# Kernel tuning notes

Measured on AMD Instinct MI355X. Metric: run time of the kernel, lower is better.

The kernel has to match this reference:

```python
import jax, jax.numpy as jnp
import numpy as np

D = 4096
K = 128
N = 8192
EPS = 1e-6


def setup_inputs() -> dict:
    key = jax.random.key(0)
    k1, k2 = jax.random.split(key)
    x = jax.random.normal(k1, (N, D), dtype=jnp.float32)
    # theta = [W (d*K), mu (d), sigma (d), alpha (K)]; sigma/alpha must be positive
    theta = jax.random.uniform(k2, (D * K + 2 * D + K,), dtype=jnp.float32)
    return {"x": x, "theta": theta, "full_data_size": 100000}


def reference(x, theta, full_data_size):
    W = theta[: D * K].reshape(D, K)
    mu = theta[D * K : D * K + D]
    sigma = theta[D * K + D : D * K + 2 * D]
    alpha = theta[D * K + 2 * D :]

    # W_multiplied = W * alpha (broadcast over columns)
    Wm = W * alpha  # [D, K]
    # var_noise = sigma * eye(D) + eps : diag(sigma) plus eps added to EVERY entry
    cov = Wm @ Wm.T + jnp.diag(sigma) + EPS  # [D, D]

    L = jnp.linalg.cholesky(cov)  # [D, D], lower
    diff = x - mu  # [N, D]
    # Solve L y = diff^T for all samples at once
    y = jax.scipy.linalg.solve_triangular(L, diff.T, lower=True)  # [D, N]
    quad = jnp.sum(y * y, axis=0)  # [N]
    logdet = 2.0 * jnp.sum(jnp.log(jnp.diagonal(L)))
    log2pi = jnp.float32(np.log(2.0 * np.pi))
    logp = -0.5 * (D * log2pi + logdet + quad)  # [N]

    n = x.shape[0]
    return jnp.sum(logp) * (full_data_size / n)
```

## Files before the change

### kernel.cpp

```cpp
#include <hip/hip_runtime.h>
#include <math.h>

#define D 4096
#define K 128
#define KP 129
#define NC 144
#define NROWS 8192
#define QS 144
#define MS 132
#define NP 132
#define NPS 136
#define NB 12
#define NPAN (NP / NB)
#define MSPLIT 6
#define LOG2PI 1.8378770664093453

typedef __attribute__((ext_vector_type(8))) short bh8;
typedef __attribute__((ext_vector_type(4))) float f32x4;

__device__ __forceinline__ unsigned short f2bf(float f) {
  unsigned int u = __float_as_uint(f);
  unsigned int r = u + 0x7FFFu + ((u >> 16) & 1u);
  return (unsigned short)(r >> 16);
}
__device__ __forceinline__ float bf2f(unsigned short u) {
  return __uint_as_float(((unsigned int)u) << 16);
}
__device__ __forceinline__ float blo(unsigned int v) { return __uint_as_float(v << 16); }
__device__ __forceinline__ float bhi(unsigned int v) { return __uint_as_float(v & 0xFFFF0000u); }

__device__ __forceinline__ float blockReduceSum256(float v) {
  #pragma unroll
  for (int off = 32; off > 0; off >>= 1) v += __shfl_down(v, off, 64);
  __shared__ float tmp[4];
  __syncthreads();
  if ((threadIdx.x & 63) == 0) tmp[threadIdx.x >> 6] = v;
  __syncthreads();
  float r = 0.0f;
  if (threadIdx.x == 0) r = tmp[0] + tmp[1] + tmp[2] + tmp[3];
  return r;
}

__global__ __launch_bounds__(256) void k_prep(const float* __restrict__ theta,
                                              unsigned short* __restrict__ VbT) {
  int c = blockIdx.x;
  const float* sg = theta + (size_t)D * K + D;
  float al = (c < K) ? theta[(size_t)D * K + 2 * D + c] : 0.0f;
  for (int d = threadIdx.x; d < D; d += 256) {
    float v;
    if (c < K)       v = theta[(size_t)d * K + c] * al / sg[d];
    else if (c == K) v = 1.0e-3f / sg[d];
    else             v = 0.0f;
    VbT[(size_t)c * D + d] = f2bf(v);
  }
}

__global__ __launch_bounds__(256) void k_M(const float* __restrict__ theta,
                                           const unsigned short* __restrict__ VbT,
                                           float* __restrict__ M) {
  int j = blockIdx.x, kk2 = blockIdx.y;
  if (kk2 < j) return;
  const float* sg = theta + (size_t)D * K + D;
  float acc = 0.0f;
  for (int d0 = threadIdx.x * 8; d0 < D; d0 += 2048) {
    uint4 ua = *reinterpret_cast<const uint4*>(&VbT[(size_t)j * D + d0]);
    uint4 ub = *reinterpret_cast<const uint4*>(&VbT[(size_t)kk2 * D + d0]);
    float4 s0 = *reinterpret_cast<const float4*>(&sg[d0]);
    float4 s1 = *reinterpret_cast<const float4*>(&sg[d0 + 4]);
    acc += s0.x * blo(ua.x) * blo(ub.x) + s0.y * bhi(ua.x) * bhi(ub.x)
         + s0.z * blo(ua.y) * blo(ub.y) + s0.w * bhi(ua.y) * bhi(ub.y)
         + s1.x * blo(ua.z) * blo(ub.z) + s1.y * bhi(ua.z) * bhi(ub.z)
         + s1.z * blo(ua.w) * blo(ub.w) + s1.w * bhi(ua.w) * bhi(ub.w);
  }
  float r = blockReduceSum256(acc);
  if (threadIdx.x == 0) {
    float m = r + (j == kk2 ? 1.0f : 0.0f);
    M[j * MS + kk2] = m;
    M[kk2 * MS + j] = m;
  }
}

__global__ __launch_bounds__(256) void k_small(const float* __restrict__ theta,
                                               const unsigned short* __restrict__ VbT,
                                               const float* __restrict__ colsum,
                                               const float* __restrict__ colsumsq,
                                               float* __restrict__ tvec,
                                               float* __restrict__ mvec,
                                               float* __restrict__ scalars) {
  int b = blockIdx.x;
  if (b < 2 * KP) {
    int c = (b >= KP) ? b - KP : b;
    const float* src = (b >= KP) ? (theta + (size_t)D * K) : colsum;
    float a = 0.0f;
    for (int d = threadIdx.x; d < D; d += 256) a += bf2f(VbT[(size_t)c * D + d]) * src[d];
    float r = blockReduceSum256(a);
    if (threadIdx.x == 0) { if (b < KP) tvec[c] = r; else mvec[c] = r; }
  } else {
    const float* mu = theta + (size_t)D * K;
    const float* sg = theta + (size_t)D * K + D;
    float a = 0.0f, bb = 0.0f;
    for (int d = threadIdx.x; d < D; d += 256) {
      float s = sg[d];
      float m = mu[d];
      a += logf(s);
      bb += (colsumsq[d] - 2.0f * m * colsum[d] + (float)NROWS * m * m) / s;
    }
    float ra = blockReduceSum256(a);
    float rb = blockReduceSum256(bb);
    if (threadIdx.x == 0) { scalars[0] = ra; scalars[1] = rb; }
  }
}

#define GBM 32
#define GBK 128
#define NSTEP (D / GBK)
#define XSS 136
#define GEMM_BLOCKS (NROWS / GBM)
#define CS_BLOCKS 32
#define CS_ROWS (NROWS / CS_BLOCKS)

struct CholSh {
  float A[NP][NPS];
  float G[NP][NPS];
  float Tst[NPAN][NB][NB + 1];
};
struct GemmSh {
  unsigned short Xs[GBM][XSS];
  unsigned short Vs[NC][XSS];
};
union ParSh {
  CholSh c;
  GemmSh g;
};

__device__ void chol_body(CholSh& sh, const float* __restrict__ Mg,
                          float* __restrict__ Gg, float* __restrict__ scalars) {
  auto& A = sh.A;
  auto& G = sh.G;
  auto& Tst = sh.Tst;
  __shared__ float redB[16];
  int tid = threadIdx.x;

  if (tid == 0) scalars[3] = 0.0f;
  for (int idx = tid; idx < NP * NP; idx += 1024) {
    int r = idx / NP, c = idx - r * NP;
    A[r][c] = (r < KP && c < KP) ? Mg[r * MS + c] : (r == c ? 1.0f : 0.0f);
  }
  __syncthreads();

  for (int p = 0; p < NPAN; ++p) {
    int j0 = p * NB, j1 = j0 + NB;
    int nbrows = NP - j1;
    int nG = p * NB;
    if (tid < 128) {
      float T[NB][NB];
      #pragma unroll
      for (int r = 0; r < NB; ++r)
        #pragma unroll
        for (int c = 0; c <= r; ++c)
          T[r][c] = A[j0 + r][j0 + c];
      float dinv[NB];
      #pragma unroll
      for (int jj = 0; jj < NB; ++jj) {
        float dv = sqrtf(T[jj][jj]);
        float iv = 1.0f / dv;
        dinv[jj] = iv;
        #pragma unroll
        for (int r = jj + 1; r < NB; ++r) T[r][jj] *= iv;
        #pragma unroll
        for (int cc = jj + 1; cc < NB; ++cc)
          #pragma unroll
          for (int r = cc; r < NB; ++r)
            T[r][cc] -= T[r][jj] * T[cc][jj];
      }
      #pragma unroll
      for (int r = 0; r < NB; ++r) {
        float tmp[NB];
        #pragma unroll
        for (int c = 0; c < r; ++c) {
          float s = 0.0f;
          #pragma unroll
          for (int k = c; k < r; ++k) s += T[r][k] * T[k][c];
          tmp[c] = -s * dinv[r];
        }
        #pragma unroll
        for (int c = 0; c < r; ++c) T[r][c] = tmp[c];
        T[r][r] = dinv[r];
      }
      if (tid == 0) {
        #pragma unroll
        for (int r = 0; r < NB; ++r) {
          float g[NB];
          #pragma unroll
          for (int c = 0; c < NB; ++c) g[c] = (c <= r) ? T[r][c] : 0.0f;
          float4* dst = reinterpret_cast<float4*>(&G[j0 + r][j0]);
          float4 g0 = {g[0], g[1], g[2], g[3]};
          float4 g1 = {g[4], g[5], g[6], g[7]};
          float4 g2 = {g[8], g[9], g[10], g[11]};
          dst[0] = g0; dst[1] = g1; dst[2] = g2;
        }
      }
      if (tid < nbrows) {
        int r = j1 + tid;
        float* arow = &A[r][j0];
        float4 q0 = *reinterpret_cast<const float4*>(arow);
        float4 q1 = *reinterpret_cast<const float4*>(arow + 4);
        float4 q2 = *reinterpret_cast<const float4*>(arow + 8);
        float ro[NB] = {q0.x, q0.y, q0.z, q0.w, q1.x, q1.y, q1.z, q1.w,
                        q2.x, q2.y, q2.z, q2.w};
        float rn[NB];
        #pragma unroll
        for (int cc = 0; cc < NB; ++cc) {
          float s = 0.0f;
          #pragma unroll
          for (int k = 0; k <= cc; ++k) s += ro[k] * T[cc][k];
          rn[cc] = s;
        }
        float4 w0 = {rn[0], rn[1], rn[2], rn[3]};
        float4 w1 = {rn[4], rn[5], rn[6], rn[7]};
        float4 w2 = {rn[8], rn[9], rn[10], rn[11]};
        *reinterpret_cast<float4*>(arow) = w0;
        *reinterpret_cast<float4*>(arow + 4) = w1;
        *reinterpret_cast<float4*>(arow + 8) = w2;
      }
    } else if (tid < 128 + MSPLIT * nG) {
      int t2 = tid - 128;
      int q = t2 / (NB * MSPLIT);
      int rem = t2 - q * (NB * MSPLIT);
      int j = rem % NB, mg = rem / NB;
      int qI = q * NB;
      int m0 = mg * 2;
      float t0 = 0.0f, t1 = 0.0f;
      for (int k = q; k < p; ++k) {
        int kI = k * NB;
        #pragma unroll
        for (int n = 0; n < NB; ++n) {
          float g = G[kI + n][qI + j];
          t0 += A[j0 + m0 + 0][kI + n] * g;
          t1 += A[j0 + m0 + 1][kI + n] * g;
        }
      }
      Tst[q][m0 + 0][j] = t0;
      Tst[q][m0 + 1][j] = t1;
    }
    __syncthreads();
    if (tid < nG) {
      int q = tid / NB, j = tid - (tid / NB) * NB;
      int qI = q * NB;
      float w[NB];
      #pragma unroll
      for (int m = 0; m < NB; ++m) w[m] = Tst[q][m][j];
      #pragma unroll
      for (int i = 0; i < NB; ++i) {
        float s = 0.0f;
        #pragma unroll
        for (int m = 0; m <= i; ++m) s += G[j0 + i][j0 + m] * w[m];
        G[j0 + i][qI + j] = -s;
      }
    } else {
      int nt = nbrows / 4;
      int ntasks = nt * (nt + 1) / 2;
      int nthr = 1024 - nG;
      for (int t = tid - nG; t < ntasks; t += nthr) {
        int r4 = (int)((sqrtf(8.0f * (float)t + 1.0f) - 1.0f) * 0.5f);
        while ((r4 + 1) * (r4 + 2) / 2 <= t) ++r4;
        while (r4 * (r4 + 1) / 2 > t) --r4;
        int c4 = t - r4 * (r4 + 1) / 2;
        int r = j1 + r4 * 4, c = j1 + c4 * 4;
        float pr[4][NB], pc[4][NB];
        #pragma unroll
        for (int i = 0; i < 4; ++i) {
          float4 a0 = *reinterpret_cast<const float4*>(&A[r + i][j0]);
          float4 a1 = *reinterpret_cast<const float4*>(&A[r + i][j0 + 4]);
          float4 a2 = *reinterpret_cast<const float4*>(&A[r + i][j0 + 8]);
          pr[i][0] = a0.x; pr[i][1] = a0.y; pr[i][2] = a0.z; pr[i][3] = a0.w;
          pr[i][4] = a1.x; pr[i][5] = a1.y; pr[i][6] = a1.z; pr[i][7] = a1.w;
          pr[i][8] = a2.x; pr[i][9] = a2.y; pr[i][10] = a2.z; pr[i][11] = a2.w;
          float4 b0 = *reinterpret_cast<const float4*>(&A[c + i][j0]);
          float4 b1 = *reinterpret_cast<const float4*>(&A[c + i][j0 + 4]);
          float4 b2 = *reinterpret_cast<const float4*>(&A[c + i][j0 + 8]);
          pc[i][0] = b0.x; pc[i][1] = b0.y; pc[i][2] = b0.z; pc[i][3] = b0.w;
          pc[i][4] = b1.x; pc[i][5] = b1.y; pc[i][6] = b1.z; pc[i][7] = b1.w;
          pc[i][8] = b2.x; pc[i][9] = b2.y; pc[i][10] = b2.z; pc[i][11] = b2.w;
        }
        float4 av[4];
        #pragma unroll
        for (int i = 0; i < 4; ++i)
          av[i] = *reinterpret_cast<const float4*>(&A[r + i][c]);
        #pragma unroll
        for (int k = 0; k < NB; ++k) {
          #pragma unroll
          for (int i = 0; i < 4; ++i) {
            av[i].x -= pr[i][k] * pc[0][k];
            av[i].y -= pr[i][k] * pc[1][k];
            av[i].z -= pr[i][k] * pc[2][k];
            av[i].w -= pr[i][k] * pc[3][k];
          }
        }
        #pragma unroll
        for (int i = 0; i < 4; ++i)
          *reinterpret_cast<float4*>(&A[r + i][c]) = av[i];
      }
    }
    __syncthreads();
  }

  for (int idx = tid; idx < NP * NP; idx += 1024) {
    int r = idx / NP, c = idx - r * NP;
    Gg[idx] = G[r][c];
  }

  float lg = (tid < NP) ? logf(G[tid][tid]) : 0.0f;
  #pragma unroll
  for (int off = 32; off > 0; off >>= 1) lg += __shfl_down(lg, off, 64);
  __syncthreads();
  if ((tid & 63) == 0) redB[tid >> 6] = lg;
  __syncthreads();
  if (tid == 0) {
    float sgl = 0.0f;
    #pragma unroll
    for (int i = 0; i < 16; ++i) sgl += redB[i];
    scalars[2] = -2.0f * sgl;
  }
}

__device__ void gemm_body(GemmSh& sh, const float* __restrict__ x,
                          const unsigned short* __restrict__ VbT,
                          unsigned short* __restrict__ Yb, int blk) {
  auto& Xs = sh.Xs;
  auto& Vs = sh.Vs;
  int tid = threadIdx.x;
  int row0 = blk * GBM;
  int wid = tid >> 6, lane = tid & 63;
  int lr = lane & 15, lk = (lane >> 4) * 8;
  int rt = wid & 1;
  int cg = wid >> 1;
  int ct0 = (cg == 0) ? 0 : (cg * 2 + 1);
  int nct = (cg == 0) ? 3 : 2;

  int sxr = tid >> 4;
  int sxk = (tid & 15) * 8;
  int vrb = tid >> 4;
  int vk  = (tid & 15) * 8;

  float4 xr0, xr1;
  uint4 vr0, vr1, vr2, vr3, vr4;
  {
    const float* xb = &x[(size_t)(row0 + sxr) * D + sxk];
    xr0 = *reinterpret_cast<const float4*>(xb);
    xr1 = *reinterpret_cast<const float4*>(xb + 4);
    const unsigned short* vb = &VbT[(size_t)vrb * D + vk];
    vr0 = *reinterpret_cast<const uint4*>(vb);
    vr1 = *reinterpret_cast<const uint4*>(vb + (size_t)32 * D);
    vr2 = *reinterpret_cast<const uint4*>(vb + (size_t)64 * D);
    vr3 = *reinterpret_cast<const uint4*>(vb + (size_t)96 * D);
    if (tid < 256) vr4 = *reinterpret_cast<const uint4*>(vb + (size_t)128 * D);
  }

  f32x4 acc0 = {0, 0, 0, 0}, acc1 = {0, 0, 0, 0}, acc2 = {0, 0, 0, 0};

  for (int s = 0; s < NSTEP; ++s) {
    {
      uint4 w;
      w.x = (unsigned)f2bf(xr0.x) | ((unsigned)f2bf(xr0.y) << 16);
      w.y = (unsigned)f2bf(xr0.z) | ((unsigned)f2bf(xr0.w) << 16);
      w.z = (unsigned)f2bf(xr1.x) | ((unsigned)f2bf(xr1.y) << 16);
      w.w = (unsigned)f2bf(xr1.z) | ((unsigned)f2bf(xr1.w) << 16);
      *reinterpret_cast<uint4*>(&Xs[sxr][sxk]) = w;
      unsigned short* vd = &Vs[vrb][vk];
      *reinterpret_cast<uint4*>(vd) = vr0;
      *reinterpret_cast<uint4*>(vd + 32 * XSS) = vr1;
      *reinterpret_cast<uint4*>(vd + 64 * XSS) = vr2;
      *reinterpret_cast<uint4*>(vd + 96 * XSS) = vr3;
      if (tid < 256) *reinterpret_cast<uint4*>(vd + 128 * XSS) = vr4;
    }
    __syncthreads();
    if (s + 1 < NSTEP) {
      const float* xb = &x[(size_t)(row0 + sxr) * D + (s + 1) * GBK + sxk];
      xr0 = *reinterpret_cast<const float4*>(xb);
      xr1 = *reinterpret_cast<const float4*>(xb + 4);
      const unsigned short* vb = &VbT[(size_t)vrb * D + (s + 1) * GBK + vk];
      vr0 = *reinterpret_cast<const uint4*>(vb);
      vr1 = *reinterpret_cast<const uint4*>(vb + (size_t)32 * D);
      vr2 = *reinterpret_cast<const uint4*>(vb + (size_t)64 * D);
      vr3 = *reinterpret_cast<const uint4*>(vb + (size_t)96 * D);
      if (tid < 256) vr4 = *reinterpret_cast<const uint4*>(vb + (size_t)128 * D);
    }
    #pragma unroll
    for (int ks = 0; ks < 4; ++ks) {
      bh8 a = *reinterpret_cast<const bh8*>(&Xs[rt * 16 + lr][ks * 32 + lk]);
      bh8 b0 = *reinterpret_cast<const bh8*>(&Vs[ct0 * 16 + lr][ks * 32 + lk]);
      acc0 = __builtin_amdgcn_mfma_f32_16x16x32_bf16(a, b0, acc0, 0, 0, 0);
      bh8 b1 = *reinterpret_cast<const bh8*>(&Vs[(ct0 + 1) * 16 + lr][ks * 32 + lk]);
      acc1 = __builtin_amdgcn_mfma_f32_16x16x32_bf16(a, b1, acc1, 0, 0, 0);
      if (nct == 3) {
        bh8 b2 = *reinterpret_cast<const bh8*>(&Vs[(ct0 + 2) * 16 + lr][ks * 32 + lk]);
        acc2 = __builtin_amdgcn_mfma_f32_16x16x32_bf16(a, b2, acc2, 0, 0, 0);
      }
    }
    __syncthreads();
  }

  int rw = row0 + rt * 16 + ((lane >> 4) << 2);
  #pragma unroll
  for (int g = 0; g < 4; ++g)
    Yb[(size_t)(rw + g) * NC + ct0 * 16 + lr] = f2bf(acc0[g]);
  #pragma unroll
  for (int g = 0; g < 4; ++g)
    Yb[(size_t)(rw + g) * NC + (ct0 + 1) * 16 + lr] = f2bf(acc1[g]);
  if (nct == 3) {
    #pragma unroll
    for (int g = 0; g < 4; ++g)
      Yb[(size_t)(rw + g) * NC + (ct0 + 2) * 16 + lr] = f2bf(acc2[g]);
  }
}

__device__ void colstats_body(const float* __restrict__ x,
                              float* __restrict__ colsum,
                              float* __restrict__ colsumsq, int cb) {
  int d4 = threadIdx.x;
  int i0 = cb * CS_ROWS;
  float4 s1 = {0, 0, 0, 0}, s2 = {0, 0, 0, 0};
  for (int i = i0; i < i0 + CS_ROWS; ++i) {
    float4 v = *reinterpret_cast<const float4*>(&x[(size_t)i * D + d4 * 4]);
    s1.x += v.x; s1.y += v.y; s1.z += v.z; s1.w += v.w;
    s2.x += v.x * v.x; s2.y += v.y * v.y; s2.z += v.z * v.z; s2.w += v.w * v.w;
  }
  atomicAdd(&colsum[d4 * 4 + 0], s1.x); atomicAdd(&colsum[d4 * 4 + 1], s1.y);
  atomicAdd(&colsum[d4 * 4 + 2], s1.z); atomicAdd(&colsum[d4 * 4 + 3], s1.w);
  atomicAdd(&colsumsq[d4 * 4 + 0], s2.x); atomicAdd(&colsumsq[d4 * 4 + 1], s2.y);
  atomicAdd(&colsumsq[d4 * 4 + 2], s2.z); atomicAdd(&colsumsq[d4 * 4 + 3], s2.w);
}

__global__ __launch_bounds__(1024, 1) void k_par(const float* __restrict__ x,
                                                 const unsigned short* __restrict__ VbT,
                                                 unsigned short* __restrict__ Yb,
                                                 const float* __restrict__ Mg,
                                                 float* __restrict__ Gg,
                                                 float* __restrict__ scalars,
                                                 float* __restrict__ colsum,
                                                 float* __restrict__ colsumsq) {
  __shared__ ParSh sh;
  int b = blockIdx.x;
  if (b == 0) {
    chol_body(sh.c, Mg, Gg, scalars);
  } else if (b <= GEMM_BLOCKS) {
    if (threadIdx.x >= 512) return;
    gemm_body(sh.g, x, VbT, Yb, b - 1);
  } else {
    colstats_body(x, colsum, colsumsq, b - 1 - GEMM_BLOCKS);
  }
}

#define SYRK_ZSPLIT 16
__global__ __launch_bounds__(256) void k_syrk(const unsigned short* __restrict__ Yb,
                                              float* __restrict__ Q) {
  int bj = blockIdx.x * 16, bk = blockIdx.y * 16;
  if (bk < bj) return;
  __shared__ float Ya[64][17];
  __shared__ float Yc[64][17];
  int i0base = blockIdx.z * (NROWS / SYRK_ZSPLIT);
  int tid = threadIdx.x;
  int tj = tid & 15, tk = tid >> 4;
  int lr = tid >> 2, lc = (tid & 3) * 4;
  float acc = 0.0f;
  for (int i0 = i0base; i0 < i0base + NROWS / SYRK_ZSPLIT; i0 += 64) {
    ushort4 va = *reinterpret_cast<const ushort4*>(&Yb[(size_t)(i0 + lr) * NC + bj + lc]);
    ushort4 vc = *reinterpret_cast<const ushort4*>(&Yb[(size_t)(i0 + lr) * NC + bk + lc]);
    Ya[lr][lc + 0] = bf2f(va.x); Ya[lr][lc + 1] = bf2f(va.y);
    Ya[lr][lc + 2] = bf2f(va.z); Ya[lr][lc + 3] = bf2f(va.w);
    Yc[lr][lc + 0] = bf2f(vc.x); Yc[lr][lc + 1] = bf2f(vc.y);
    Yc[lr][lc + 2] = bf2f(vc.z); Yc[lr][lc + 3] = bf2f(vc.w);
    __syncthreads();
    #pragma unroll
    for (int ii = 0; ii < 64; ++ii) acc += Ya[ii][tj] * Yc[ii][tk];
    __syncthreads();
  }
  atomicAdd(&Q[(bj + tj) * QS + bk + tk], acc);
  if (bj != bk) atomicAdd(&Q[(bk + tk) * QS + bj + tj], acc);
}

__global__ __launch_bounds__(256) void k_trace(const float* __restrict__ Gg,
                                               const float* __restrict__ Qg,
                                               const float* __restrict__ tvec,
                                               const float* __restrict__ mvec,
                                               float* __restrict__ scalars) {
  int bj = blockIdx.x * 16, bk = blockIdx.y * 16;
  if (bk < bj) return;
  int tj = threadIdx.x & 15, tk = threadIdx.x >> 4;
  int j = bj + tj, k = bk + tk;
  float acc = 0.0f;
  if (j <= k && k < NP) {
    float h0 = 0.f, h1 = 0.f;
    int i = k;
    for (; i + 1 < NP; i += 2) {
      h0 += Gg[(size_t)i * NP + j] * Gg[(size_t)i * NP + k];
      h1 += Gg[(size_t)(i + 1) * NP + j] * Gg[(size_t)(i + 1) * NP + k];
    }
    for (; i < NP; ++i) h0 += Gg[(size_t)i * NP + j] * Gg[(size_t)i * NP + k];
    float h = h0 + h1;
    float S = 0.0f;
    if (j < KP && k < KP) {
      float tlj = tvec[j], mlj = mvec[j], tlk = tvec[k], mlk = mvec[k];
      S = Qg[j * QS + k] - tlj * mlk - mlj * tlk + (float)NROWS * mlj * mlk;
    }
    acc = ((j == k) ? 1.0f : 2.0f) * h * S;
  }
  float r = blockReduceSum256(acc);
  if (threadIdx.x == 0) atomicAdd(&scalars[3], r);
}

__global__ void k_combine(const float* __restrict__ scalars,
                          const int* __restrict__ fds,
                          float* __restrict__ out) {
  if (threadIdx.x == 0) {
    double sumlog  = (double)scalars[0];
    double term1   = (double)scalars[1];
    double logdetM = (double)scalars[2];
    double tr      = (double)scalars[3];
    double total = (double)NROWS * (double)D * LOG2PI
                 + (double)NROWS * (sumlog + logdetM)
                 + term1 - tr;
    double scale = (double)fds[0] / (double)NROWS;
    out[0] = (float)(scale * (-0.5) * total);
  }
}

extern "C" void kernel_launch(void* const* d_in, const int* in_sizes, int n_in,
                              void* d_out, int out_size, void* d_ws, size_t ws_size,
                              hipStream_t stream) {
  const float* x     = (const float*)d_in[0];
  const float* theta = (const float*)d_in[1];
  const int*   fds   = (const int*)d_in[2];
  float* out = (float*)d_out;
  char* ws = (char*)d_ws;

  unsigned short* Yb  = (unsigned short*)ws;
  unsigned short* VbT = (unsigned short*)(ws + 2359296);
  float* Q        = (float*)(ws + 2359296 + 1179648);
  float* colsum   = (float*)(ws + 2359296 + 1179648 + 82944);
  float* colsumsq = colsum + D;
  float* M        = colsumsq + D;
  float* tvec     = M + KP * MS;
  float* mvec     = tvec + MS;
  float* scalars  = mvec + MS;
  float* Gg       = scalars + 8;

  hipMemsetAsync(Q, 0, (size_t)(QS * QS + 2 * D) * sizeof(float), stream);

  k_prep   <<<dim3(NC), 256, 0, stream>>>(theta, VbT);
  k_M      <<<dim3(KP, KP), 256, 0, stream>>>(theta, VbT, M);
  k_par    <<<dim3(1 + GEMM_BLOCKS + CS_BLOCKS), 1024, 0, stream>>>(
               x, VbT, Yb, M, Gg, scalars, colsum, colsumsq);
  k_syrk   <<<dim3(QS / 16, QS / 16, SYRK_ZSPLIT), 256, 0, stream>>>(Yb, Q);
  k_small  <<<dim3(2 * KP + 1), 256, 0, stream>>>(theta, VbT, colsum, colsumsq,
                                                  tvec, mvec, scalars);
  k_trace  <<<dim3(9, 9), 256, 0, stream>>>(Gg, Q, tvec, mvec, scalars);
  k_combine<<<dim3(1), 64, 0, stream>>>(scalars, fds, out);
}
```

Before: 163.7 us.

## Fuse SYRK, column stats and small reductions into the parallel GEMM kernel

The per-block Y tile is now reduced to its column sums and its Y^T Y contribution directly from shared memory and accumulated with atomics into tvec and Q. This removes the bf16 Y round-trip through global memory and the separate syrk kernel. Column statistics now compute the centered, sigma-scaled quadratic term directly. The mvec dot products move into extra k_par blocks, and the final combine is folded into k_trace through a last-block-done counter, which drops three kernel launches. In exchange it adds many global atomics (about 10K per GEMM block into Q), plus float atomic accumulation order nondeterminism.

```diff
diff --git a/kernel.cpp b/kernel.cpp
--- a/kernel.cpp
+++ b/kernel.cpp
@@ -13,6 +13,7 @@
 #define NB 12
 #define NPAN (NP / NB)
 #define MSPLIT 6
+#define NTRACE 45
 #define LOG2PI 1.8378770664093453
 
 typedef __attribute__((ext_vector_type(8))) short bh8;
@@ -38,6 +39,21 @@
   __syncthreads();
   float r = 0.0f;
   if (threadIdx.x == 0) r = tmp[0] + tmp[1] + tmp[2] + tmp[3];
+  return r;
+}
+
+__device__ __forceinline__ float blockReduceSum1024(float v) {
+  #pragma unroll
+  for (int off = 32; off > 0; off >>= 1) v += __shfl_down(v, off, 64);
+  __shared__ float tmp16[16];
+  __syncthreads();
+  if ((threadIdx.x & 63) == 0) tmp16[threadIdx.x >> 6] = v;
+  __syncthreads();
+  float r = 0.0f;
+  if (threadIdx.x == 0) {
+    #pragma unroll
+    for (int i = 0; i < 16; ++i) r += tmp16[i];
+  }
   return r;
 }
 
@@ -80,41 +96,11 @@
   }
 }
 
-__global__ __launch_bounds__(256) void k_small(const float* __restrict__ theta,
-                                               const unsigned short* __restrict__ VbT,
-                                               const float* __restrict__ colsum,
-                                               const float* __restrict__ colsumsq,
-                                               float* __restrict__ tvec,
-                                               float* __restrict__ mvec,
-                                               float* __restrict__ scalars) {
-  int b = blockIdx.x;
-  if (b < 2 * KP) {
-    int c = (b >= KP) ? b - KP : b;
-    const float* src = (b >= KP) ? (theta + (size_t)D * K) : colsum;
-    float a = 0.0f;
-    for (int d = threadIdx.x; d < D; d += 256) a += bf2f(VbT[(size_t)c * D + d]) * src[d];
-    float r = blockReduceSum256(a);
-    if (threadIdx.x == 0) { if (b < KP) tvec[c] = r; else mvec[c] = r; }
-  } else {
-    const float* mu = theta + (size_t)D * K;
-    const float* sg = theta + (size_t)D * K + D;
-    float a = 0.0f, bb = 0.0f;
-    for (int d = threadIdx.x; d < D; d += 256) {
-      float s = sg[d];
-      float m = mu[d];
-      a += logf(s);
-      bb += (colsumsq[d] - 2.0f * m * colsum[d] + (float)NROWS * m * m) / s;
-    }
-    float ra = blockReduceSum256(a);
-    float rb = blockReduceSum256(bb);
-    if (threadIdx.x == 0) { scalars[0] = ra; scalars[1] = rb; }
-  }
-}
-
 #define GBM 32
 #define GBK 128
 #define NSTEP (D / GBK)
 #define XSS 136
+#define YSS 145
 #define GEMM_BLOCKS (NROWS / GBM)
 #define CS_BLOCKS 32
 #define CS_ROWS (NROWS / CS_BLOCKS)
@@ -125,8 +111,10 @@
   float Tst[NPAN][NB][NB + 1];
 };
 struct GemmSh {
-  unsigned short Xs[GBM][XSS];
-  unsigned short Vs[NC][XSS];
+  union {
+    struct { unsigned short Xs[GBM][XSS]; unsigned short Vs[NC][XSS]; } io;
+    float Ys[GBM][YSS];
+  } u;
 };
 union ParSh {
   CholSh c;
@@ -141,7 +129,6 @@
   __shared__ float redB[16];
   int tid = threadIdx.x;
 
-  if (tid == 0) scalars[3] = 0.0f;
   for (int idx = tid; idx < NP * NP; idx += 1024) {
     int r = idx / NP, c = idx - r * NP;
     A[r][c] = (r < KP && c < KP) ? Mg[r * MS + c] : (r == c ? 1.0f : 0.0f);
@@ -326,9 +313,10 @@
 
 __device__ void gemm_body(GemmSh& sh, const float* __restrict__ x,
                           const unsigned short* __restrict__ VbT,
-                          unsigned short* __restrict__ Yb, int blk) {
-  auto& Xs = sh.Xs;
-  auto& Vs = sh.Vs;
+                          float* __restrict__ tvec, float* __restrict__ Q,
+                          int blk) {
+  auto& Xs = sh.u.io.Xs;
+  auto& Vs = sh.u.io.Vs;
   int tid = threadIdx.x;
   int row0 = blk * GBM;
   int wid = tid >> 6, lane = tid & 63;
@@ -401,92 +389,112 @@
     __syncthreads();
   }
 
-  int rw = row0 + rt * 16 + ((lane >> 4) << 2);
+  int rl = rt * 16 + ((lane >> 4) << 2);
   #pragma unroll
-  for (int g = 0; g < 4; ++g)
-    Yb[(size_t)(rw + g) * NC + ct0 * 16 + lr] = f2bf(acc0[g]);
+  for (int g = 0; g < 4; ++g) sh.u.Ys[rl + g][ct0 * 16 + lr] = acc0[g];
   #pragma unroll
-  for (int g = 0; g < 4; ++g)
-    Yb[(size_t)(rw + g) * NC + (ct0 + 1) * 16 + lr] = f2bf(acc1[g]);
+  for (int g = 0; g < 4; ++g) sh.u.Ys[rl + g][(ct0 + 1) * 16 + lr] = acc1[g];
   if (nct == 3) {
     #pragma unroll
-    for (int g = 0; g < 4; ++g)
-      Yb[(size_t)(rw + g) * NC + (ct0 + 2) * 16 + lr] = f2bf(acc2[g]);
+    for (int g = 0; g < 4; ++g) sh.u.Ys[rl + g][(ct0 + 2) * 16 + lr] = acc2[g];
+  }
+  __syncthreads();
+
+  if (tid < NC) {
+    float s = 0.0f;
+    #pragma unroll 8
+    for (int r = 0; r < GBM; ++r) s += sh.u.Ys[r][tid];
+    atomicAdd(&tvec[tid], s);
+  }
+  for (int t = tid; t < NC * (NC + 1) / 2; t += 512) {
+    int k = (int)((sqrtf(8.0f * (float)t + 1.0f) - 1.0f) * 0.5f);
+    while ((k + 1) * (k + 2) / 2 <= t) ++k;
+    while (k * (k + 1) / 2 > t) --k;
+    int j = t - k * (k + 1) / 2;
+    float s0 = 0.f, s1 = 0.f;
+    #pragma unroll 4
+    for (int r = 0; r < GBM; r += 2) {
+      s0 += sh.u.Ys[r][j] * sh.u.Ys[r][k];
+      s1 += sh.u.Ys[r + 1][j] * sh.u.Ys[r + 1][k];
+    }
+    atomicAdd(&Q[j * QS + k], s0 + s1);
   }
 }
 
 __device__ void colstats_body(const float* __restrict__ x,
-                              float* __restrict__ colsum,
-                              float* __restrict__ colsumsq, int cb) {
+                              const float* __restrict__ theta,
+                              float* __restrict__ scalars, int cb) {
   int d4 = threadIdx.x;
   int i0 = cb * CS_ROWS;
-  float4 s1 = {0, 0, 0, 0}, s2 = {0, 0, 0, 0};
+  const float* mu = theta + (size_t)D * K;
+  const float* sg = mu + D;
+  float4 mu4 = *reinterpret_cast<const float4*>(&mu[d4 * 4]);
+  float4 sg4 = *reinterpret_cast<const float4*>(&sg[d4 * 4]);
+  float4 iv = {1.0f / sg4.x, 1.0f / sg4.y, 1.0f / sg4.z, 1.0f / sg4.w};
+  float t1 = 0.0f;
   for (int i = i0; i < i0 + CS_ROWS; ++i) {
     float4 v = *reinterpret_cast<const float4*>(&x[(size_t)i * D + d4 * 4]);
-    s1.x += v.x; s1.y += v.y; s1.z += v.z; s1.w += v.w;
-    s2.x += v.x * v.x; s2.y += v.y * v.y; s2.z += v.z * v.z; s2.w += v.w * v.w;
-  }
-  atomicAdd(&colsum[d4 * 4 + 0], s1.x); atomicAdd(&colsum[d4 * 4 + 1], s1.y);
-  atomicAdd(&colsum[d4 * 4 + 2], s1.z); atomicAdd(&colsum[d4 * 4 + 3], s1.w);
-  atomicAdd(&colsumsq[d4 * 4 + 0], s2.x); atomicAdd(&colsumsq[d4 * 4 + 1], s2.y);
-  atomicAdd(&colsumsq[d4 * 4 + 2], s2.z); atomicAdd(&colsumsq[d4 * 4 + 3], s2.w);
+    float dx = v.x - mu4.x, dy = v.y - mu4.y, dz = v.z - mu4.z, dw = v.w - mu4.w;
+    t1 += dx * dx * iv.x + dy * dy * iv.y + dz * dz * iv.z + dw * dw * iv.w;
+  }
+  float r = blockReduceSum1024(t1);
+  if (threadIdx.x == 0) atomicAdd(&scalars[1], r);
+  if (cb == 0) {
+    float lg = logf(sg4.x) + logf(sg4.y) + logf(sg4.z) + logf(sg4.w);
+    float r2 = blockReduceSum1024(lg);
+    if (threadIdx.x == 0) atomicAdd(&scalars[0], r2);
+  }
+}
+
+__device__ void mvec_body(const unsigned short* __restrict__ VbT,
+                          const float* __restrict__ theta,
+                          float* __restrict__ mvec, int c) {
+  const float* mu = theta + (size_t)D * K;
+  int d = threadIdx.x * 4;
+  ushort4 uv = *reinterpret_cast<const ushort4*>(&VbT[(size_t)c * D + d]);
+  float4 m4 = *reinterpret_cast<const float4*>(&mu[d]);
+  float a = bf2f(uv.x) * m4.x + bf2f(uv.y) * m4.y
+          + bf2f(uv.z) * m4.z + bf2f(uv.w) * m4.w;
+  float r = blockReduceSum1024(a);
+  if (threadIdx.x == 0) mvec[c] = r;
 }
 
 __global__ __launch_bounds__(1024, 1) void k_par(const float* __restrict__ x,
+                                                 const float* __restrict__ theta,
                                                  const unsigned short* __restrict__ VbT,
-                                                 unsigned short* __restrict__ Yb,
                                                  const float* __restrict__ Mg,
                                                  float* __restrict__ Gg,
                                                  float* __restrict__ scalars,
-                                                 float* __restrict__ colsum,
-                                                 float* __restrict__ colsumsq) {
+                                                 float* __restrict__ tvec,
+                                                 float* __restrict__ Q,
+                                                 float* __restrict__ mvec) {
   __shared__ ParSh sh;
   int b = blockIdx.x;
   if (b == 0) {
     chol_body(sh.c, Mg, Gg, scalars);
   } else if (b <= GEMM_BLOCKS) {
     if (threadIdx.x >= 512) return;
-    gemm_body(sh.g, x, VbT, Yb, b - 1);
+    gemm_body(sh.g, x, VbT, tvec, Q, b - 1);
+  } else if (b <= GEMM_BLOCKS + CS_BLOCKS) {
+    colstats_body(x, theta, scalars, b - 1 - GEMM_BLOCKS);
   } else {
-    colstats_body(x, colsum, colsumsq, b - 1 - GEMM_BLOCKS);
-  }
-}
-
-#define SYRK_ZSPLIT 16
-__global__ __launch_bounds__(256) void k_syrk(const unsigned short* __restrict__ Yb,
-                                              float* __restrict__ Q) {
-  int bj = blockIdx.x * 16, bk = blockIdx.y * 16;
-  if (bk < bj) return;
-  __shared__ float Ya[64][17];
-  __shared__ float Yc[64][17];
-  int i0base = blockIdx.z * (NROWS / SYRK_ZSPLIT);
-  int tid = threadIdx.x;
-  int tj = tid & 15, tk = tid >> 4;
-  int lr = tid >> 2, lc = (tid & 3) * 4;
-  float acc = 0.0f;
-  for (int i0 = i0base; i0 < i0base + NROWS / SYRK_ZSPLIT; i0 += 64) {
-    ushort4 va = *reinterpret_cast<const ushort4*>(&Yb[(size_t)(i0 + lr) * NC + bj + lc]);
-    ushort4 vc = *reinterpret_cast<const ushort4*>(&Yb[(size_t)(i0 + lr) * NC + bk + lc]);
-    Ya[lr][lc + 0] = bf2f(va.x); Ya[lr][lc + 1] = bf2f(va.y);
-    Ya[lr][lc + 2] = bf2f(va.z); Ya[lr][lc + 3] = bf2f(va.w);
-    Yc[lr][lc + 0] = bf2f(vc.x); Yc[lr][lc + 1] = bf2f(vc.y);
-    Yc[lr][lc + 2] = bf2f(vc.z); Yc[lr][lc + 3] = bf2f(vc.w);
-    __syncthreads();
-    #pragma unroll
-    for (int ii = 0; ii < 64; ++ii) acc += Ya[ii][tj] * Yc[ii][tk];
-    __syncthreads();
-  }
-  atomicAdd(&Q[(bj + tj) * QS + bk + tk], acc);
-  if (bj != bk) atomicAdd(&Q[(bk + tk) * QS + bj + tj], acc);
+    mvec_body(VbT, theta, mvec, b - 1 - GEMM_BLOCKS - CS_BLOCKS);
+  }
 }
 
 __global__ __launch_bounds__(256) void k_trace(const float* __restrict__ Gg,
                                                const float* __restrict__ Qg,
                                                const float* __restrict__ tvec,
                                                const float* __restrict__ mvec,
-                                               float* __restrict__ scalars) {
-  int bj = blockIdx.x * 16, bk = blockIdx.y * 16;
-  if (bk < bj) return;
+                                               float* __restrict__ scalars,
+                                               const int* __restrict__ fds,
+                                               float* __restrict__ out) {
+  int b = blockIdx.x;
+  int tkT = (int)((sqrtf(8.0f * (float)b + 1.0f) - 1.0f) * 0.5f);
+  while ((tkT + 1) * (tkT + 2) / 2 <= b) ++tkT;
+  while (tkT * (tkT + 1) / 2 > b) --tkT;
+  int tjT = b - tkT * (tkT + 1) / 2;
+  int bj = tjT * 16, bk = tkT * 16;
   int tj = threadIdx.x & 15, tk = threadIdx.x >> 4;
   int j = bj + tj, k = bk + tk;
   float acc = 0.0f;
@@ -507,22 +515,21 @@
     acc = ((j == k) ? 1.0f : 2.0f) * h * S;
   }
   float r = blockReduceSum256(acc);
-  if (threadIdx.x == 0) atomicAdd(&scalars[3], r);
-}
-
-__global__ void k_combine(const float* __restrict__ scalars,
-                          const int* __restrict__ fds,
-                          float* __restrict__ out) {
   if (threadIdx.x == 0) {
-    double sumlog  = (double)scalars[0];
-    double term1   = (double)scalars[1];
-    double logdetM = (double)scalars[2];
-    double tr      = (double)scalars[3];
-    double total = (double)NROWS * (double)D * LOG2PI
-                 + (double)NROWS * (sumlog + logdetM)
-                 + term1 - tr;
-    double scale = (double)fds[0] / (double)NROWS;
-    out[0] = (float)(scale * (-0.5) * total);
+    atomicAdd(&scalars[3], r);
+    __threadfence();
+    unsigned old = atomicAdd(reinterpret_cast<unsigned int*>(scalars + 4), 1u);
+    if (old == NTRACE - 1) {
+      float tr = atomicAdd(&scalars[3], 0.0f);
+      double sumlog  = (double)scalars[0];
+      double term1   = (double)scalars[1];
+      double logdetM = (double)scalars[2];
+      double total = (double)NROWS * (double)D * LOG2PI
+                   + (double)NROWS * (sumlog + logdetM)
+                   + term1 - (double)tr;
+      double scale = (double)fds[0] / (double)NROWS;
+      out[0] = (float)(scale * (-0.5) * total);
+    }
   }
 }
 
@@ -533,28 +540,21 @@
   const float* theta = (const float*)d_in[1];
   const int*   fds   = (const int*)d_in[2];
   float* out = (float*)d_out;
-  char* ws = (char*)d_ws;
-
-  unsigned short* Yb  = (unsigned short*)ws;
-  unsigned short* VbT = (unsigned short*)(ws + 2359296);
-  float* Q        = (float*)(ws + 2359296 + 1179648);
-  float* colsum   = (float*)(ws + 2359296 + 1179648 + 82944);
-  float* colsumsq = colsum + D;
-  float* M        = colsumsq + D;
-  float* tvec     = M + KP * MS;
-  float* mvec     = tvec + MS;
-  float* scalars  = mvec + MS;
-  float* Gg       = scalars + 8;
-
-  hipMemsetAsync(Q, 0, (size_t)(QS * QS + 2 * D) * sizeof(float), stream);
-
-  k_prep   <<<dim3(NC), 256, 0, stream>>>(theta, VbT);
-  k_M      <<<dim3(KP, KP), 256, 0, stream>>>(theta, VbT, M);
-  k_par    <<<dim3(1 + GEMM_BLOCKS + CS_BLOCKS), 1024, 0, stream>>>(
-               x, VbT, Yb, M, Gg, scalars, colsum, colsumsq);
-  k_syrk   <<<dim3(QS / 16, QS / 16, SYRK_ZSPLIT), 256, 0, stream>>>(Yb, Q);
-  k_small  <<<dim3(2 * KP + 1), 256, 0, stream>>>(theta, VbT, colsum, colsumsq,
-                                                  tvec, mvec, scalars);
-  k_trace  <<<dim3(9, 9), 256, 0, stream>>>(Gg, Q, tvec, mvec, scalars);
-  k_combine<<<dim3(1), 64, 0, stream>>>(scalars, fds, out);
-}
+  float* ws = (float*)d_ws;
+
+  float* Q        = ws;
+  float* tvec     = Q + QS * QS;
+  float* scalars  = tvec + NC;
+  unsigned short* VbT = (unsigned short*)(scalars + 8);
+  float* M        = (float*)(VbT + (size_t)NC * D);
+  float* mvec     = M + KP * MS;
+  float* Gg       = mvec + NC;
+
+  hipMemsetAsync(Q, 0, (size_t)(QS * QS + NC + 8) * sizeof(float), stream);
+
+  k_prep <<<dim3(NC), 256, 0, stream>>>(theta, VbT);
+  k_M    <<<dim3(KP, KP), 256, 0, stream>>>(theta, VbT, M);
+  k_par  <<<dim3(1 + GEMM_BLOCKS + CS_BLOCKS + KP), 1024, 0, stream>>>(
+             x, theta, VbT, M, Gg, scalars, tvec, Q, mvec);
+  k_trace<<<dim3(NTRACE), 256, 0, stream>>>(Gg, Q, tvec, mvec, scalars, fds, out);
+}
```

New measurement: 369.7 us. 126% more time.
